# Kernel optimization log

Measured on AMD Instinct MI355X. Metric: run time of the kernel, lower is better.

Reference implementation:

```python
import jax, jax.numpy as jnp
import numpy as np

MD = 4  # max displacement -> (2*MD+1)**2 = 81 output channels

def setup_inputs() -> dict:
    key = jax.random.key(0)
    k1, k2 = jax.random.split(key)
    B, C, H, W = 4, 128, 128, 256
    t1 = jax.random.normal(k1, (B, C, H, W), dtype=jnp.float32)
    t2 = jax.random.normal(k2, (B, C, H, W), dtype=jnp.float32)
    return {"t1": t1, "t2": t2}

def reference(t1, t2):
    # PWC-Net correlation: for each displacement (dy,dx) in [-MD,MD]^2,
    # corr[b, d, y, x] = mean_c t1[b,c,y,x] * t2[b,c,y+dy,x+dx]
    B, C, H, W = t1.shape
    t2p = jnp.pad(t2, ((0, 0), (0, 0), (MD, MD), (MD, MD)))
    outs = []
    for dy in range(2 * MD + 1):
        for dx in range(2 * MD + 1):
            shifted = t2p[:, :, dy:dy + H, dx:dx + W]  # (B,C,H,W)
            outs.append(jnp.mean(t1 * shifted, axis=1))  # (B,H,W)
    return jnp.stack(outs, axis=1)  # (B, 81, H, W)
```

## Files before the change

kernel.cpp:

```cpp
#include <hip/hip_runtime.h>

#define MD   4
#define B_   4
#define C_   128
#define H_   128
#define W_   256
#define ND   9
#define NW   9
#define XPT  8

typedef float float4v __attribute__((ext_vector_type(4)));

__global__ __launch_bounds__(NW * 64, 3)
void corr_kernel(const float* __restrict__ t1,
                 const float* __restrict__ t2,
                 float* __restrict__ out) {
    const int tid  = threadIdx.x;
    const int lane = tid & 63;
    const int w    = tid >> 6;
    const int bid  = blockIdx.x;
    const int swz  = (bid & 7) * 32 + (bid >> 3);
    const int yp   = swz & 63;
    const int b    = swz >> 6;
    const int y0   = yp * 2;
    const int half = lane >> 5;
    const int lx   = lane & 31;
    const int x0   = lx * XPT;
    const int yrow = y0 + half;
    const int yy   = yrow + w - MD;
    const bool live = (0 <= yy) && (yy < H_);
    const int  yc  = yy < 0 ? 0 : (yy > H_ - 1 ? H_ - 1 : yy);
    const float sc = live ? (1.0f / (float)C_) : 0.0f;
    const bool lm  = (lx == 0);
    const bool rm  = (lx == 31);

    float acc[ND][XPT];
    #pragma unroll
    for (int dx = 0; dx < ND; ++dx)
        #pragma unroll
        for (int j = 0; j < XPT; ++j) acc[dx][j] = 0.0f;

    const float* p1 = t1 + (((size_t)(b * C_)) * H_ + yrow) * W_ + x0;
    const float* p2 = t2 + (((size_t)(b * C_)) * H_ + yc  ) * W_ + x0;
    const size_t chstr = (size_t)H_ * W_;

    for (int c = 0; c < C_; ++c) {
        const float4v a0 = *(const float4v*)(p1 + (size_t)c * chstr);
        const float4v a1 = *(const float4v*)(p1 + (size_t)c * chstr + 4);
        const float4v v0 = *(const float4v*)(p2 + (size_t)c * chstr);
        const float4v v1 = *(const float4v*)(p2 + (size_t)c * chstr + 4);

        float win[XPT + 2 * MD];
        #pragma unroll
        for (int k = 0; k < 4; ++k) {
            const float up = __shfl_up(v1[k], 1);
            const float dn = __shfl_down(v0[k], 1);
            win[k]      = lm ? 0.0f : up;
            win[4 + k]  = v0[k];
            win[8 + k]  = v1[k];
            win[12 + k] = rm ? 0.0f : dn;
        }

        #pragma unroll
        for (int dx = 0; dx < ND; ++dx)
            #pragma unroll
            for (int j = 0; j < XPT; ++j) {
                const float aj = (j < 4) ? a0[j] : a1[j - 4];
                acc[dx][j] = fmaf(aj, win[dx + j], acc[dx][j]);
            }
    }

    #pragma unroll
    for (int dx = 0; dx < ND; ++dx) {
        float4v o0, o1;
        #pragma unroll
        for (int j = 0; j < 4; ++j) {
            o0[j] = acc[dx][j]     * sc;
            o1[j] = acc[dx][4 + j] * sc;
        }
        const size_t oidx =
            (((size_t)(b * ND * ND) + w * ND + dx) * H_ + yrow) * W_ + x0;
        *(float4v*)&out[oidx]     = o0;
        *(float4v*)&out[oidx + 4] = o1;
    }
}

extern "C" void kernel_launch(void* const* d_in, const int* in_sizes, int n_in,
                              void* d_out, int out_size, void* d_ws, size_t ws_size,
                              hipStream_t stream) {
    const float* t1 = (const float*)d_in[0];
    const float* t2 = (const float*)d_in[1];
    float* out      = (float*)d_out;
    corr_kernel<<<dim3(B_ * H_ / 2), NW * 64, 0, stream>>>(t1, t2, out);
}
```

Measured before the change: 77.97 us.

## Stage shared t1 rows in LDS via double-buffered async global-to-LDS loads

All nine waves of a block read the same two t1 rows for every channel, so each row was fetched from global memory nine times over. The kernel now copies chunks of 16 channels of t1 into a double-buffered LDS tile with global_load_lds, prefetching the next chunk while computing the current one. Waves then read t1 from LDS and keep reading t2 from global memory. The tile takes 64KB of LDS per block, which may lower occupancy below the launch-bounds target of three blocks per CU, and it adds a block barrier per chunk.

Result: slower. 89.33 us (+14.6%).

```diff
diff --git a/kernel.cpp b/kernel.cpp
--- a/kernel.cpp
+++ b/kernel.cpp
@@ -8,6 +8,8 @@
 #define ND   9
 #define NW   9
 #define XPT  8
+#define CHK  16
+#define NCHK (C_ / CHK)
 
 typedef float float4v __attribute__((ext_vector_type(4)));
 
@@ -15,6 +17,8 @@
 void corr_kernel(const float* __restrict__ t1,
                  const float* __restrict__ t2,
                  float* __restrict__ out) {
+    __shared__ __align__(16) float t1s[2][CHK][2][W_];
+
     const int tid  = threadIdx.x;
     const int lane = tid & 63;
     const int w    = tid >> 6;
@@ -40,34 +44,58 @@
         #pragma unroll
         for (int j = 0; j < XPT; ++j) acc[dx][j] = 0.0f;
 
-    const float* p1 = t1 + (((size_t)(b * C_)) * H_ + yrow) * W_ + x0;
-    const float* p2 = t2 + (((size_t)(b * C_)) * H_ + yc  ) * W_ + x0;
+    const float* p2 = t2 + (((size_t)(b * C_)) * H_ + yc) * W_ + x0;
     const size_t chstr = (size_t)H_ * W_;
 
-    for (int c = 0; c < C_; ++c) {
-        const float4v a0 = *(const float4v*)(p1 + (size_t)c * chstr);
-        const float4v a1 = *(const float4v*)(p1 + (size_t)c * chstr + 4);
-        const float4v v0 = *(const float4v*)(p2 + (size_t)c * chstr);
-        const float4v v1 = *(const float4v*)(p2 + (size_t)c * chstr + 4);
+    auto STAGE = [&](int buf, int k) {
+        const int c0 = k * CHK;
+        for (int s = w; s < 2 * CHK; s += NW) {
+            const int ch  = s >> 1;
+            const int row = s & 1;
+            const float* src =
+                t1 + (((size_t)(b * C_ + c0 + ch)) * H_ + (y0 + row)) * W_ + lane * 4;
+            __builtin_amdgcn_global_load_lds(
+                (const __attribute__((address_space(1))) unsigned int*)src,
+                (__attribute__((address_space(3))) unsigned int*)&t1s[buf][ch][row][0],
+                16, 0, 0);
+        }
+    };
 
-        float win[XPT + 2 * MD];
-        #pragma unroll
-        for (int k = 0; k < 4; ++k) {
-            const float up = __shfl_up(v1[k], 1);
-            const float dn = __shfl_down(v0[k], 1);
-            win[k]      = lm ? 0.0f : up;
-            win[4 + k]  = v0[k];
-            win[8 + k]  = v1[k];
-            win[12 + k] = rm ? 0.0f : dn;
+    STAGE(0, 0);
+    __syncthreads();
+
+    for (int k = 0; k < NCHK; ++k) {
+        const int buf = k & 1;
+        if (k + 1 < NCHK) STAGE(buf ^ 1, k + 1);
+        const int c0 = k * CHK;
+
+        #pragma unroll 2
+        for (int ch = 0; ch < CHK; ++ch) {
+            const float4v a0 = *(const float4v*)&t1s[buf][ch][half][x0];
+            const float4v a1 = *(const float4v*)&t1s[buf][ch][half][x0 + 4];
+            const float4v v0 = *(const float4v*)(p2 + (size_t)(c0 + ch) * chstr);
+            const float4v v1 = *(const float4v*)(p2 + (size_t)(c0 + ch) * chstr + 4);
+
+            float win[XPT + 2 * MD];
+            #pragma unroll
+            for (int q = 0; q < 4; ++q) {
+                const float up = __shfl_up(v1[q], 1);
+                const float dn = __shfl_down(v0[q], 1);
+                win[q]      = lm ? 0.0f : up;
+                win[4 + q]  = v0[q];
+                win[8 + q]  = v1[q];
+                win[12 + q] = rm ? 0.0f : dn;
+            }
+
+            #pragma unroll
+            for (int dx = 0; dx < ND; ++dx)
+                #pragma unroll
+                for (int j = 0; j < XPT; ++j) {
+                    const float aj = (j < 4) ? a0[j] : a1[j - 4];
+                    acc[dx][j] = fmaf(aj, win[dx + j], acc[dx][j]);
+                }
         }
-
-        #pragma unroll
-        for (int dx = 0; dx < ND; ++dx)
-            #pragma unroll
-            for (int j = 0; j < XPT; ++j) {
-                const float aj = (j < 4) ? a0[j] : a1[j - 4];
-                acc[dx][j] = fmaf(aj, win[dx + j], acc[dx][j]);
-            }
+        __syncthreads();
     }
 
     #pragma unroll
```
